# Kernel optimization log

Measured on AMD Instinct MI355X. Metric: run time of the kernel, lower is better.

## Reference

```python
import jax, jax.numpy as jnp
import numpy as np

N_HEAD, CTX, N_EMBD, HEAD_SIZE = 16, 2048, 1024, 64
D_MODEL = N_HEAD * HEAD_SIZE  # 1024


def setup_inputs() -> dict:
    key = jax.random.key(0)
    ks = jax.random.split(key, 8)
    s_in = 1.0 / np.sqrt(N_EMBD)
    s_d = 1.0 / np.sqrt(D_MODEL)
    s_ff = 1.0 / np.sqrt(4 * D_MODEL)
    return {
        "x": jax.random.normal(ks[0], (4, CTX, N_EMBD), dtype=jnp.float32),
        # per-head q/k/v projections stacked over heads: [H, n_embd, head_size]
        "Wq": jax.random.normal(ks[1], (N_HEAD, N_EMBD, HEAD_SIZE), dtype=jnp.float32) * s_in,
        "Wk": jax.random.normal(ks[2], (N_HEAD, N_EMBD, HEAD_SIZE), dtype=jnp.float32) * s_in,
        "Wv": jax.random.normal(ks[3], (N_HEAD, N_EMBD, HEAD_SIZE), dtype=jnp.float32) * s_in,
        # FFN: Linear(d, 4d) -> Linear(4d, d) -> ReLU (dropout = identity in eval)
        "W1": jax.random.normal(ks[4], (D_MODEL, 4 * D_MODEL), dtype=jnp.float32) * s_d,
        "b1": jnp.zeros((4 * D_MODEL,), dtype=jnp.float32),
        "W2": jax.random.normal(ks[5], (4 * D_MODEL, D_MODEL), dtype=jnp.float32) * s_ff,
        "b2": jnp.zeros((D_MODEL,), dtype=jnp.float32),
    }


def reference(x, Wq, Wk, Wv, W1, b1, W2, b2):
    B, T, C = x.shape
    scale = 1.0 / np.sqrt(HEAD_SIZE)
    # project: [B,T,C] x [H,C,D] -> [B,H,T,D]
    q = jnp.einsum('btc,hcd->bhtd', x, Wq)
    k = jnp.einsum('btc,hcd->bhtd', x, Wk)
    v = jnp.einsum('btc,hcd->bhtd', x, Wv)
    # causal attention scores [B,H,T,T]
    wei = jnp.einsum('bhtd,bhsd->bhts', q, k) * scale
    causal = jnp.tril(jnp.ones((T, T), dtype=bool))
    wei = jnp.where(causal, wei, -jnp.inf)
    wei = jax.nn.softmax(wei, axis=-1)
    out = jnp.einsum('bhts,bhsd->bhtd', wei, v)
    # concat heads -> [B,T,H*D]
    out = out.transpose(0, 2, 1, 3).reshape(B, T, D_MODEL)
    # FFN: note original applies ReLU AFTER the second linear
    h = out @ W1 + b1
    h = h @ W2 + b2
    return jax.nn.relu(h)
```

## Files before the change

kernel.cpp:

```cpp
#include <hip/hip_runtime.h>
#include <hip/hip_bf16.h>

typedef unsigned short u16;
typedef unsigned int u32;
typedef short bf16x8 __attribute__((ext_vector_type(8)));
typedef float floatx4 __attribute__((ext_vector_type(4)));

#define CTX 2048
#define HEADSZ 64
#define NHEAD 16
#define DMODEL 1024
#define DFF 4096
#define MROWS 8192
#define C_SCALE 0.18033688011112042f

__device__ __forceinline__ u16 f2b(float f) {
  union { float f; u32 i; } x; x.f = f;
  u32 i = x.i;
  return (u16)((i + 0x7fffu + ((i >> 16) & 1u)) >> 16);
}
__device__ __forceinline__ u32 pack2(float a, float b) {
  return (u32)f2b(a) | ((u32)f2b(b) << 16);
}
__device__ __forceinline__ u32 cvtpk(float a, float b) {
  u32 r;
  asm("v_cvt_pk_bf16_f32 %0, %1, %2" : "=v"(r) : "v"(a), "v"(b));
  return r;
}

__device__ __forceinline__ void gl2lds16(const u16* g, u16* l) {
  __builtin_amdgcn_global_load_lds(
      (const __attribute__((address_space(1))) void*)g,
      (__attribute__((address_space(3))) void*)l, 16, 0, 0);
}

__global__ __launch_bounds__(256) void cvt_f32_bf16(const float* __restrict__ in,
                                                    u16* __restrict__ out) {
  int i = (blockIdx.x * 256 + threadIdx.x) * 4;
  float4 v = *(const float4*)(in + i);
  *(uint2*)(out + i) = make_uint2(pack2(v.x, v.y), pack2(v.z, v.w));
}

__global__ void transpose_f32_bf16(const float* __restrict__ in, u16* __restrict__ out,
                                   int R, int C, long ibs, long obs) {
  __shared__ u16 tile[32][33];
  const float* ip = in + (size_t)blockIdx.z * ibs;
  u16* op = out + (size_t)blockIdx.z * obs;
  int c0 = blockIdx.x * 32, r0 = blockIdx.y * 32;
  int tx = threadIdx.x, ty = threadIdx.y;
#pragma unroll
  for (int i = 0; i < 32; i += 8)
    tile[ty + i][tx] = f2b(ip[(size_t)(r0 + ty + i) * C + (c0 + tx)]);
  __syncthreads();
#pragma unroll
  for (int i = 0; i < 32; i += 8)
    op[(size_t)(c0 + ty + i) * R + (r0 + tx)] = tile[tx][ty + i];
}

__global__ void transpose_qkv(const float* __restrict__ Wq, const float* __restrict__ Wk,
                              const float* __restrict__ Wv, u16* __restrict__ out) {
  __shared__ u16 tile[32][33];
  int z = blockIdx.z;
  int sec = z >> 4, hh = z & 15;
  const float* ip = (sec == 0 ? Wq : sec == 1 ? Wk : Wv) + (size_t)hh * 65536;
  u16* op = out + (size_t)(sec * 16 + hh) * 65536;
  int c0 = blockIdx.x * 32, r0 = blockIdx.y * 32;
  int tx = threadIdx.x, ty = threadIdx.y;
#pragma unroll
  for (int i = 0; i < 32; i += 8)
    tile[ty + i][tx] = f2b(ip[(size_t)(r0 + ty + i) * 64 + (c0 + tx)]);
  __syncthreads();
#pragma unroll
  for (int i = 0; i < 32; i += 8)
    op[(size_t)(c0 + ty + i) * 1024 + (r0 + tx)] = tile[tx][ty + i];
}

__global__ __launch_bounds__(256) void reduce_wf(const float* __restrict__ p,
                                                 u16* __restrict__ wft) {
  int i = (blockIdx.x * 256 + threadIdx.x) * 4;
  float4 s = *(const float4*)(p + i);
#pragma unroll
  for (int sp = 1; sp < 8; sp++) {
    float4 v = *(const float4*)(p + ((size_t)sp << 20) + i);
    s.x += v.x; s.y += v.y; s.z += v.z; s.w += v.w;
  }
  *(uint2*)(wft + i) = make_uint2(pack2(s.x, s.y), pack2(s.z, s.w));
}

__global__ __launch_bounds__(256) void bf_init(const float* __restrict__ b2,
                                               float* __restrict__ bf) {
  int n = blockIdx.x * 256 + threadIdx.x;
  bf[n] = b2[n];
}
__global__ __launch_bounds__(256) void bf_acc(const float* __restrict__ b1,
                                              const float* __restrict__ W2,
                                              float* __restrict__ bf) {
  int n = blockIdx.x * 256 + threadIdx.x;
  int f0 = blockIdx.y * 128;
  float s = 0.f;
  for (int f = 0; f < 128; f++) s += b1[f0 + f] * W2[(size_t)(f0 + f) * 1024 + n];
  atomicAdd(&bf[n], s);
}

template <int MODE>
__global__ __launch_bounds__(512, 2) void gemm128(
    const u16* __restrict__ A, const u16* __restrict__ Bt,
    const float* __restrict__ bias,
    void* __restrict__ o0v, void* __restrict__ o1v, void* __restrict__ o2v,
    int N, int Klen, int Kstride) {
  __shared__ __align__(16) u16 As[3][8192];
  __shared__ __align__(16) u16 Bs[3][16384];
  const int tid = threadIdx.x;
  const int quad = (tid >> 4) & 3, l15 = tid & 15;
  const int wave = tid >> 6;
  const int wr = wave >> 2, wc = wave & 3;

  const int id = blockIdx.x;
  int blockM, blockN, koff;
  if (MODE == 3) {
    blockM = (id & 7) << 7;
    blockN = ((id >> 3) & 3) << 8;
    koff = (id >> 5) << 9;
  } else {
    blockM = (((id & 7) << 3) | ((id >> 3) & 7)) << 7;
    blockN = (id >> 6) << 8;
    koff = 0;
  }

  const int sub = tid >> 3;
  const int kslot = (tid & 7) ^ (sub & 7);
  const int rA = blockM + ((sub >> 5) << 6) + (sub & 31);
  const u16* a0 = A + (size_t)(rA + 0) * Kstride + koff + kslot * 8;
  const u16* a1 = A + (size_t)(rA + 32) * Kstride + koff + kslot * 8;
  const int rB = blockN + sub;
  const u16* b0 = Bt + (size_t)(rB + 0) * Kstride + koff + kslot * 8;
  const u16* b1 = Bt + (size_t)(rB + 64) * Kstride + koff + kslot * 8;
  const u16* b2 = Bt + (size_t)(rB + 128) * Kstride + koff + kslot * 8;
  const u16* b3 = Bt + (size_t)(rB + 192) * Kstride + koff + kslot * 8;

  const int arow = ((wr << 5) + l15) << 7;
  const int brow = ((wc << 6) + l15) << 7;
  const int swz0 = (quad ^ (l15 & 7)) << 4;
  const int swz1 = ((4 + quad) ^ (l15 & 7)) << 4;

  floatx4 acc[4][4];
#pragma unroll
  for (int i = 0; i < 4; i++)
#pragma unroll
    for (int j = 0; j < 4; j++) acc[i][j] = (floatx4){0.f, 0.f, 0.f, 0.f};

  const int nk = Klen >> 6;

  gl2lds16(a0, &As[0][tid * 8]);
  gl2lds16(a1, &As[0][4096 + tid * 8]);
  gl2lds16(b0, &Bs[0][0 * 4096 + tid * 8]);
  gl2lds16(b1, &Bs[0][1 * 4096 + tid * 8]);
  gl2lds16(b2, &Bs[0][2 * 4096 + tid * 8]);
  gl2lds16(b3, &Bs[0][3 * 4096 + tid * 8]);
  gl2lds16(a0 + 64, &As[1][tid * 8]);
  gl2lds16(a1 + 64, &As[1][4096 + tid * 8]);
  gl2lds16(b0 + 64, &Bs[1][0 * 4096 + tid * 8]);
  gl2lds16(b1 + 64, &Bs[1][1 * 4096 + tid * 8]);
  gl2lds16(b2 + 64, &Bs[1][2 * 4096 + tid * 8]);
  gl2lds16(b3 + 64, &Bs[1][3 * 4096 + tid * 8]);
  asm volatile("s_waitcnt vmcnt(6)" ::: "memory");
  __builtin_amdgcn_s_barrier();
  a0 += 128; a1 += 128;
  b0 += 128; b1 += 128; b2 += 128; b3 += 128;

#define MFMA_Q(q, arq)                                                         \
  _Pragma("unroll") for (int nf = 0; nf < 4; nf++)                             \
    acc[q][nf] = __builtin_amdgcn_mfma_f32_16x16x32_bf16(                      \
        arq[0], br[nf][0], acc[q][nf], 0, 0, 0);                               \
  _Pragma("unroll") for (int nf = 0; nf < 4; nf++)                             \
    acc[q][nf] = __builtin_amdgcn_mfma_f32_16x16x32_bf16(                      \
        arq[1], br[nf][1], acc[q][nf], 0, 0, 0);

  int cur = 0;
#pragma unroll 1
  for (int t = 0; t < nk; t++) {
    const char* ab = (const char*)As[cur];
    const char* bb = (const char*)Bs[cur];
    int nxt = cur + 2; if (nxt >= 3) nxt -= 3;
    u16* An = As[nxt];
    u16* Bn = Bs[nxt];
    const bool st2 = (t + 2 < nk);
    bf16x8 br[4][2], ar0[2], ar1[2], ar2[2], ar3[2];

#pragma unroll
    for (int nf = 0; nf < 4; nf++) {
      br[nf][0] = *(const bf16x8*)(bb + nf * 2048 + brow + swz0);
      br[nf][1] = *(const bf16x8*)(bb + nf * 2048 + brow + swz1);
    }
    ar0[0] = *(const bf16x8*)(ab + arow + swz0);
    ar0[1] = *(const bf16x8*)(ab + arow + swz1);
    ar1[0] = *(const bf16x8*)(ab + 2048 + arow + swz0);
    ar1[1] = *(const bf16x8*)(ab + 2048 + arow + swz1);
    if (st2) {
      gl2lds16(a0, An + tid * 8);
      gl2lds16(a1, An + 4096 + tid * 8);
      gl2lds16(b0, Bn + 0 * 4096 + tid * 8);
      gl2lds16(b1, Bn + 1 * 4096 + tid * 8);
      gl2lds16(b2, Bn + 2 * 4096 + tid * 8);
      gl2lds16(b3, Bn + 3 * 4096 + tid * 8);
    }
    __builtin_amdgcn_s_barrier();
    asm volatile("s_waitcnt lgkmcnt(0)" ::: "memory");
    __builtin_amdgcn_s_setprio(1);
    MFMA_Q(0, ar0)
    MFMA_Q(1, ar1)
    __builtin_amdgcn_s_setprio(0);
    __builtin_amdgcn_s_barrier();

    ar2[0] = *(const bf16x8*)(ab + 8192 + arow + swz0);
    ar2[1] = *(const bf16x8*)(ab + 8192 + arow + swz1);
    ar3[0] = *(const bf16x8*)(ab + 8192 + 2048 + arow + swz0);
    ar3[1] = *(const bf16x8*)(ab + 8192 + 2048 + arow + swz1);
    __builtin_amdgcn_s_barrier();
    asm volatile("s_waitcnt lgkmcnt(0)" ::: "memory");
    __builtin_amdgcn_s_setprio(1);
    MFMA_Q(2, ar2)
    MFMA_Q(3, ar3)
    __builtin_amdgcn_s_setprio(0);
    if (st2)
      asm volatile("s_waitcnt vmcnt(6)" ::: "memory");
    else
      asm volatile("s_waitcnt vmcnt(0)" ::: "memory");
    __builtin_amdgcn_s_barrier();

    a0 += 64; a1 += 64;
    b0 += 64; b1 += 64; b2 += 64; b3 += 64;
    cur = (cur == 2) ? 0 : cur + 1;
  }
#undef MFMA_Q

  const int m0 = blockM + wr * 64 + quad * 4;
  const int n0 = blockN + wc * 64 + l15;
  if (MODE == 0) {
    u16* o0 = (u16*)o0v; u16* o1 = (u16*)o1v; u16* o2 = (u16*)o2v;
    const int lane = tid & 63;
    const int n0w = blockN + wc * 64;
    const int sec = n0w >> 10, hh = (n0w >> 6) & 15;
    const int m0w = blockM + wr * 64;
    const int b = m0w >> 11, t0 = m0w & 2047;
    const int lr = lane >> 3, lc = lane & 7;
    u16* buf = (u16*)Bs[0] + wave * 4096;
    if (sec < 2) {
      u16* dst = (sec == 0) ? o0 : o1;
      const float scl = (sec == 0) ? C_SCALE : 1.0f;
#pragma unroll
      for (int nf = 0; nf < 4; nf++)
#pragma unroll
        for (int mf = 0; mf < 4; mf++)
#pragma unroll
          for (int r = 0; r < 4; r++) {
            int row = mf * 16 + quad * 4 + r;
            int col2 = (nf * 16 + l15) ^ ((row & 7) << 3);
            buf[row * 64 + col2] = f2b(acc[mf][nf][r] * scl);
          }
      u16* base = dst + ((size_t)((b * 16 + hh) * 2048 + t0)) * 64 + lc * 8;
#pragma unroll
      for (int i = 0; i < 8; i++) {
        int row = i * 8 + lr;
        uint4 v = *(const uint4*)(buf + row * 64 + ((lc ^ lr) << 3));
        *(uint4*)(base + (size_t)row * 64) = v;
      }
    } else {
      u16* dstv = o2 + ((size_t)((b * 16 + hh) * 64)) * CTX + t0;
#pragma unroll
      for (int nf = 0; nf < 4; nf++)
#pragma unroll
        for (int mf = 0; mf < 4; mf++) {
          int dr = nf * 16 + l15;
          int tc = (mf * 16 + quad * 4) ^ ((dr & 7) << 3);
          *(uint2*)&buf[dr * 64 + tc] = make_uint2(
              pack2(acc[mf][nf][0], acc[mf][nf][1]),
              pack2(acc[mf][nf][2], acc[mf][nf][3]));
        }
#pragma unroll
      for (int i = 0; i < 8; i++) {
        int dr = i * 8 + lr;
        uint4 v = *(const uint4*)&buf[dr * 64 + ((lc * 8) ^ ((dr & 7) << 3))];
        *(uint4*)(dstv + (size_t)dr * CTX + lc * 8) = v;
      }
    }
  } else if (MODE == 2) {
    float* o0 = (float*)o0v;
#pragma unroll
    for (int nf = 0; nf < 4; nf++) {
      int n = n0 + nf * 16;
      float bv = bias[n];
#pragma unroll
      for (int mf = 0; mf < 4; mf++)
#pragma unroll
        for (int r = 0; r < 4; r++) {
          int m = m0 + mf * 16 + r;
          float v = acc[mf][nf][r] + bv;
          o0[(size_t)m * N + n] = v > 0.f ? v : 0.f;
        }
    }
  } else {
    float* o0 = (float*)o0v + ((size_t)(id >> 5) << 20);
#pragma unroll
    for (int nf = 0; nf < 4; nf++) {
      int n = n0 + nf * 16;
#pragma unroll
      for (int mf = 0; mf < 4; mf++)
#pragma unroll
        for (int r = 0; r < 4; r++) {
          int m = m0 + mf * 16 + r;
          o0[(size_t)m * N + n] = acc[mf][nf][r];
        }
    }
  }
}

__global__ __launch_bounds__(256) void attn_mfma(
    const u16* __restrict__ Q, const u16* __restrict__ K,
    const u16* __restrict__ Vt, u16* __restrict__ out) {
  __shared__ __align__(16) u16 Kbuf[2][4096];
  __shared__ __align__(16) u16 Vbuf[2][4096];
  __shared__ __align__(16) u16 Plds[4][32][72];
  const int tid = threadIdx.x;
  const int wave = tid >> 6, lane = tid & 63;
  const int quad = lane >> 4, l15 = lane & 15;
  const int sx = l15 & 7;
  const int bh = blockIdx.x;
  const int j = 15 - blockIdx.y;
  const size_t qkb = (size_t)bh * CTX * 64;
  const size_t vb = (size_t)bh * 64 * CTX;

  const int ch0 = wave * 64 + lane;
  const int ch1 = 256 + ch0;
  const int r0 = ch0 >> 3, s0 = (ch0 & 7) ^ (r0 & 7);
  const int r1 = ch1 >> 3, s1 = (ch1 & 7) ^ (r1 & 7);
  const u16* kg0 = K + qkb + r0 * 64 + s0 * 8;
  const u16* kg1 = K + qkb + r1 * 64 + s1 * 8;
  const u16* vg0 = Vt + vb + (size_t)r0 * CTX + s0 * 8;
  const u16* vg1 = Vt + vb + (size_t)r1 * CTX + s1 * 8;

  const int qbase = j * 128 + wave * 32;
  const int NST = 2 * j + 2;
  const int nstw = 2 * j + (wave >> 1) + 1;

  bf16x8 qf[2][2];
#pragma unroll
  for (int mt = 0; mt < 2; mt++)
#pragma unroll
    for (int kc = 0; kc < 2; kc++)
      qf[mt][kc] = *(const bf16x8*)(Q + qkb + (size_t)(qbase + mt * 16 + l15) * 64 + kc * 32 + quad * 8);

  bf16x8 ones;
#pragma unroll
  for (int i = 0; i < 8; i++) ones[i] = (short)0x3F80;

  floatx4 o[2][4];
#pragma unroll
  for (int mt = 0; mt < 2; mt++)
#pragma unroll
    for (int dt = 0; dt < 4; dt++) o[mt][dt] = (floatx4){0.f, 0.f, 0.f, 0.f};
  floatx4 lacc[2];
  lacc[0] = (floatx4){0.f, 0.f, 0.f, 0.f};
  lacc[1] = (floatx4){0.f, 0.f, 0.f, 0.f};

  gl2lds16(kg0, &Kbuf[0][wave * 512]);
  gl2lds16(kg1, &Kbuf[0][2048 + wave * 512]);
  gl2lds16(vg0, &Vbuf[0][wave * 512]);
  gl2lds16(vg1, &Vbuf[0][2048 + wave * 512]);

#pragma unroll 1
  for (int st = 0; st < NST; st++) {
    __syncthreads();
    if (st + 1 < NST) {
      const int sb = (st + 1) * 64;
      const int b = (st + 1) & 1;
      gl2lds16(kg0 + sb * 64, &Kbuf[b][wave * 512]);
      gl2lds16(kg1 + sb * 64, &Kbuf[b][2048 + wave * 512]);
      gl2lds16(vg0 + sb, &Vbuf[b][wave * 512]);
      gl2lds16(vg1 + sb, &Vbuf[b][2048 + wave * 512]);
    }
    if (st >= nstw) continue;
    const int sbase = st * 64;
    const u16* kb = Kbuf[st & 1];
    const u16* vv = Vbuf[st & 1];

    floatx4 stf[2][4];
    __builtin_amdgcn_s_setprio(1);
#pragma unroll
    for (int sc = 0; sc < 4; sc++) {
      const bf16x8* kr = (const bf16x8*)(kb + (sc * 16 + l15) * 64);
      bf16x8 k0 = kr[quad ^ sx];
      bf16x8 k1 = kr[(4 + quad) ^ sx];
#pragma unroll
      for (int mt = 0; mt < 2; mt++) {
        floatx4 z = (floatx4){0.f, 0.f, 0.f, 0.f};
        z = __builtin_amdgcn_mfma_f32_16x16x32_bf16(k0, qf[mt][0], z, 0, 0, 0);
        stf[mt][sc] = __builtin_amdgcn_mfma_f32_16x16x32_bf16(k1, qf[mt][1], z, 0, 0, 0);
      }
    }
    __builtin_amdgcn_s_setprio(0);
    if (st == nstw - 1) {
#pragma unroll
      for (int mt = 0; mt < 2; mt++) {
        int qq = qbase + mt * 16 + l15;
#pragma unroll
        for (int sc = 0; sc < 4; sc++)
#pragma unroll
          for (int r = 0; r < 4; r++) {
            int s = sbase + sc * 16 + quad * 4 + r;
            if (s > qq) stf[mt][sc][r] = -1e30f;
          }
      }
    }
#pragma unroll
    for (int mt = 0; mt < 2; mt++) {
#pragma unroll
      for (int sc = 0; sc < 4; sc++) {
        floatx4 s4 = stf[mt][sc];
        float p0 = exp2f(s4[0]);
        float p1 = exp2f(s4[1]);
        float p2 = exp2f(s4[2]);
        float p3 = exp2f(s4[3]);
        *(uint2*)&Plds[wave][mt * 16 + l15][sc * 16 + quad * 4] =
            make_uint2(cvtpk(p0, p1), cvtpk(p2, p3));
      }
    }
    asm volatile("s_waitcnt lgkmcnt(0)" ::: "memory");
    __builtin_amdgcn_s_setprio(1);
#pragma unroll
    for (int sc2 = 0; sc2 < 2; sc2++) {
      bf16x8 pf[2];
#pragma unroll
      for (int mt = 0; mt < 2; mt++)
        pf[mt] = *(const bf16x8*)&Plds[wave][mt * 16 + l15][sc2 * 32 + quad * 8];
#pragma unroll
      for (int mt = 0; mt < 2; mt++)
        lacc[mt] = __builtin_amdgcn_mfma_f32_16x16x32_bf16(ones, pf[mt], lacc[mt], 0, 0, 0);
#pragma unroll
      for (int dt = 0; dt < 4; dt++) {
        const bf16x8* vr = (const bf16x8*)(vv + (dt * 16 + l15) * 64);
        bf16x8 vf = vr[(sc2 * 4 + quad) ^ sx];
#pragma unroll
        for (int mt = 0; mt < 2; mt++)
          o[mt][dt] = __builtin_amdgcn_mfma_f32_16x16x32_bf16(vf, pf[mt], o[mt][dt], 0, 0, 0);
      }
    }
    __builtin_amdgcn_s_setprio(0);
  }

#pragma unroll
  for (int mt = 0; mt < 2; mt++) {
    float inv = 1.0f / lacc[mt][0];
    int row = (bh >> 4) * CTX + qbase + mt * 16 + l15;
    u16* orow = out + (size_t)row * DMODEL + (bh & 15) * 64;
#pragma unroll
    for (int dt = 0; dt < 4; dt++) {
      floatx4 v = o[mt][dt];
      *(u32*)(orow + dt * 16 + quad * 4) = cvtpk(v[0] * inv, v[1] * inv);
      *(u32*)(orow + dt * 16 + quad * 4 + 2) = cvtpk(v[2] * inv, v[3] * inv);
    }
  }
}

extern "C" void kernel_launch(void* const* d_in, const int* in_sizes, int n_in,
                              void* d_out, int out_size, void* d_ws, size_t ws_size,
                              hipStream_t stream) {
  const float* x  = (const float*)d_in[0];
  const float* Wq = (const float*)d_in[1];
  const float* Wk = (const float*)d_in[2];
  const float* Wv = (const float*)d_in[3];
  const float* W1 = (const float*)d_in[4];
  const float* b1 = (const float*)d_in[5];
  const float* W2 = (const float*)d_in[6];
  const float* b2 = (const float*)d_in[7];
  float* out = (float*)d_out;

  u16* ws    = (u16*)d_ws;
  u16* W2t   = ws;
  u16* W1b   = W2t + (size_t)1024 * 4096;
  u16* Wft   = W1b + (size_t)1024 * 4096;
  float* bfv = (float*)(Wft + (size_t)1024 * 1024);
  u16* xb    = Wft + (size_t)1024 * 1024 + 4096;
  u16* Wqkvt = xb + (size_t)MROWS * 1024;
  u16* q     = Wqkvt + (size_t)3072 * 1024;
  u16* k     = q + (size_t)MROWS * 1024;
  u16* vt    = k + (size_t)MROWS * 1024;
  u16* att   = xb;
  float* partials = (float*)q;

  cvt_f32_bf16<<<MROWS * 1024 / 1024, 256, 0, stream>>>(x, xb);
  cvt_f32_bf16<<<1024 * 4096 / 1024, 256, 0, stream>>>(W1, W1b);

  dim3 tb(32, 8);
  transpose_qkv<<<dim3(2, 32, 48), tb, 0, stream>>>(Wq, Wk, Wv, Wqkvt);
  transpose_f32_bf16<<<dim3(32, 128, 1), tb, 0, stream>>>(W2, W2t, 4096, 1024, 0, 0);

  gemm128<3><<<256, 512, 0, stream>>>(W2t, W1b, nullptr, partials, nullptr, nullptr,
                                      1024, 512, 4096);
  reduce_wf<<<1024, 256, 0, stream>>>(partials, Wft);
  bf_init<<<4, 256, 0, stream>>>(b2, bfv);
  bf_acc<<<dim3(4, 32), 256, 0, stream>>>(b1, W2, bfv);

  gemm128<0><<<768, 512, 0, stream>>>(xb, Wqkvt, nullptr, q, k, vt, 3072, 1024, 1024);
  attn_mfma<<<dim3(64, 16), 256, 0, stream>>>(q, k, vt, att);
  gemm128<2><<<256, 512, 0, stream>>>(att, Wft, bfv, out, nullptr, nullptr,
                                      1024, 1024, 1024);
}
```

Before: 330.7 us.

## Shrink GEMM LDS to double-buffered K=32 tiles and merge small launches

```diff
diff --git a/kernel.cpp b/kernel.cpp
--- a/kernel.cpp
+++ b/kernel.cpp
@@ -34,11 +34,19 @@
       (__attribute__((address_space(3))) void*)l, 16, 0, 0);
 }
 
-__global__ __launch_bounds__(256) void cvt_f32_bf16(const float* __restrict__ in,
-                                                    u16* __restrict__ out) {
+__global__ __launch_bounds__(256) void cvt2(const float* __restrict__ x,
+                                            u16* __restrict__ xb,
+                                            const float* __restrict__ w1,
+                                            u16* __restrict__ w1b) {
   int i = (blockIdx.x * 256 + threadIdx.x) * 4;
-  float4 v = *(const float4*)(in + i);
-  *(uint2*)(out + i) = make_uint2(pack2(v.x, v.y), pack2(v.z, v.w));
+  if (i < MROWS * 1024) {
+    float4 v = *(const float4*)(x + i);
+    *(uint2*)(xb + i) = make_uint2(pack2(v.x, v.y), pack2(v.z, v.w));
+  } else {
+    int j = i - MROWS * 1024;
+    float4 v = *(const float4*)(w1 + j);
+    *(uint2*)(w1b + j) = make_uint2(pack2(v.x, v.y), pack2(v.z, v.w));
+  }
 }
 
 __global__ void transpose_f32_bf16(const float* __restrict__ in, u16* __restrict__ out,
@@ -87,11 +95,6 @@
   *(uint2*)(wft + i) = make_uint2(pack2(s.x, s.y), pack2(s.z, s.w));
 }
 
-__global__ __launch_bounds__(256) void bf_init(const float* __restrict__ b2,
-                                               float* __restrict__ bf) {
-  int n = blockIdx.x * 256 + threadIdx.x;
-  bf[n] = b2[n];
-}
 __global__ __launch_bounds__(256) void bf_acc(const float* __restrict__ b1,
                                               const float* __restrict__ W2,
                                               float* __restrict__ bf) {
@@ -103,13 +106,12 @@
 }
 
 template <int MODE>
-__global__ __launch_bounds__(512, 2) void gemm128(
+__global__ __launch_bounds__(512, 4) void gemm128(
     const u16* __restrict__ A, const u16* __restrict__ Bt,
     const float* __restrict__ bias,
     void* __restrict__ o0v, void* __restrict__ o1v, void* __restrict__ o2v,
     int N, int Klen, int Kstride) {
-  __shared__ __align__(16) u16 As[3][8192];
-  __shared__ __align__(16) u16 Bs[3][16384];
+  __shared__ __align__(16) u16 SH[32768];
   const int tid = threadIdx.x;
   const int quad = (tid >> 4) & 3, l15 = tid & 15;
   const int wave = tid >> 6;
@@ -127,21 +129,11 @@
     koff = 0;
   }
 
-  const int sub = tid >> 3;
-  const int kslot = (tid & 7) ^ (sub & 7);
-  const int rA = blockM + ((sub >> 5) << 6) + (sub & 31);
-  const u16* a0 = A + (size_t)(rA + 0) * Kstride + koff + kslot * 8;
-  const u16* a1 = A + (size_t)(rA + 32) * Kstride + koff + kslot * 8;
-  const int rB = blockN + sub;
-  const u16* b0 = Bt + (size_t)(rB + 0) * Kstride + koff + kslot * 8;
-  const u16* b1 = Bt + (size_t)(rB + 64) * Kstride + koff + kslot * 8;
-  const u16* b2 = Bt + (size_t)(rB + 128) * Kstride + koff + kslot * 8;
-  const u16* b3 = Bt + (size_t)(rB + 192) * Kstride + koff + kslot * 8;
-
-  const int arow = ((wr << 5) + l15) << 7;
-  const int brow = ((wc << 6) + l15) << 7;
-  const int swz0 = (quad ^ (l15 & 7)) << 4;
-  const int swz1 = ((4 + quad) ^ (l15 & 7)) << 4;
+  const int crow = tid >> 2;
+  const int cslot = (tid & 3) ^ (crow & 3);
+  const u16* ap  = A + (size_t)(blockM + crow) * Kstride + koff + cslot * 8;
+  const u16* bp0 = Bt + (size_t)(blockN + crow) * Kstride + koff + cslot * 8;
+  const u16* bp1 = bp0 + (size_t)128 * Kstride;
 
   floatx4 acc[4][4];
 #pragma unroll
@@ -149,90 +141,50 @@
 #pragma unroll
     for (int j = 0; j < 4; j++) acc[i][j] = (floatx4){0.f, 0.f, 0.f, 0.f};
 
-  const int nk = Klen >> 6;
-
-  gl2lds16(a0, &As[0][tid * 8]);
-  gl2lds16(a1, &As[0][4096 + tid * 8]);
-  gl2lds16(b0, &Bs[0][0 * 4096 + tid * 8]);
-  gl2lds16(b1, &Bs[0][1 * 4096 + tid * 8]);
-  gl2lds16(b2, &Bs[0][2 * 4096 + tid * 8]);
-  gl2lds16(b3, &Bs[0][3 * 4096 + tid * 8]);
-  gl2lds16(a0 + 64, &As[1][tid * 8]);
-  gl2lds16(a1 + 64, &As[1][4096 + tid * 8]);
-  gl2lds16(b0 + 64, &Bs[1][0 * 4096 + tid * 8]);
-  gl2lds16(b1 + 64, &Bs[1][1 * 4096 + tid * 8]);
-  gl2lds16(b2 + 64, &Bs[1][2 * 4096 + tid * 8]);
-  gl2lds16(b3 + 64, &Bs[1][3 * 4096 + tid * 8]);
-  asm volatile("s_waitcnt vmcnt(6)" ::: "memory");
-  __builtin_amdgcn_s_barrier();
-  a0 += 128; a1 += 128;
-  b0 += 128; b1 += 128; b2 += 128; b3 += 128;
-
-#define MFMA_Q(q, arq)                                                         \
-  _Pragma("unroll") for (int nf = 0; nf < 4; nf++)                             \
-    acc[q][nf] = __builtin_amdgcn_mfma_f32_16x16x32_bf16(                      \
-        arq[0], br[nf][0], acc[q][nf], 0, 0, 0);                               \
-  _Pragma("unroll") for (int nf = 0; nf < 4; nf++)                             \
-    acc[q][nf] = __builtin_amdgcn_mfma_f32_16x16x32_bf16(                      \
-        arq[1], br[nf][1], acc[q][nf], 0, 0, 0);
-
-  int cur = 0;
+  const int nk = Klen >> 5;
+
+  gl2lds16(ap, SH + tid * 8);
+  gl2lds16(bp0, SH + 8192 + tid * 8);
+  gl2lds16(bp1, SH + 8192 + 4096 + tid * 8);
+  ap += 32; bp0 += 32; bp1 += 32;
+
+  const int aoff = (wr * 64 + l15) * 64 + ((quad ^ (l15 & 3)) << 4);
+  const int boff = (wc * 64 + l15) * 64 + ((quad ^ (l15 & 3)) << 4);
+
 #pragma unroll 1
   for (int t = 0; t < nk; t++) {
-    const char* ab = (const char*)As[cur];
-    const char* bb = (const char*)Bs[cur];
-    int nxt = cur + 2; if (nxt >= 3) nxt -= 3;
-    u16* An = As[nxt];
-    u16* Bn = Bs[nxt];
-    const bool st2 = (t + 2 < nk);
-    bf16x8 br[4][2], ar0[2], ar1[2], ar2[2], ar3[2];
-
-#pragma unroll
-    for (int nf = 0; nf < 4; nf++) {
-      br[nf][0] = *(const bf16x8*)(bb + nf * 2048 + brow + swz0);
-      br[nf][1] = *(const bf16x8*)(bb + nf * 2048 + brow + swz1);
-    }
-    ar0[0] = *(const bf16x8*)(ab + arow + swz0);
-    ar0[1] = *(const bf16x8*)(ab + arow + swz1);
-    ar1[0] = *(const bf16x8*)(ab + 2048 + arow + swz0);
-    ar1[1] = *(const bf16x8*)(ab + 2048 + arow + swz1);
-    if (st2) {
-      gl2lds16(a0, An + tid * 8);
-      gl2lds16(a1, An + 4096 + tid * 8);
-      gl2lds16(b0, Bn + 0 * 4096 + tid * 8);
-      gl2lds16(b1, Bn + 1 * 4096 + tid * 8);
-      gl2lds16(b2, Bn + 2 * 4096 + tid * 8);
-      gl2lds16(b3, Bn + 3 * 4096 + tid * 8);
+    const int cur = t & 1, nxt = cur ^ 1;
+    if (t + 1 < nk) {
+      u16* An = SH + nxt * 4096;
+      u16* Bn = SH + 8192 + nxt * 8192;
+      gl2lds16(ap, An + tid * 8);
+      gl2lds16(bp0, Bn + tid * 8);
+      gl2lds16(bp1, Bn + 4096 + tid * 8);
+      ap += 32; bp0 += 32; bp1 += 32;
+      asm volatile("s_waitcnt vmcnt(3)" ::: "memory");
+    } else {
+      asm volatile("s_waitcnt vmcnt(0)" ::: "memory");
     }
     __builtin_amdgcn_s_barrier();
+    const char* ab = (const char*)(SH + cur * 4096);
+    const char* bb = (const char*)(SH + 8192 + cur * 8192);
+    bf16x8 ar[4], br[4];
+#pragma unroll
+    for (int mf = 0; mf < 4; mf++)
+      ar[mf] = *(const bf16x8*)(ab + mf * 1024 + aoff);
+#pragma unroll
+    for (int nf = 0; nf < 4; nf++)
+      br[nf] = *(const bf16x8*)(bb + nf * 1024 + boff);
     asm volatile("s_waitcnt lgkmcnt(0)" ::: "memory");
     __builtin_amdgcn_s_setprio(1);
-    MFMA_Q(0, ar0)
-    MFMA_Q(1, ar1)
+#pragma unroll
+    for (int mf = 0; mf < 4; mf++)
+#pragma unroll
+      for (int nf = 0; nf < 4; nf++)
+        acc[mf][nf] = __builtin_amdgcn_mfma_f32_16x16x32_bf16(ar[mf], br[nf], acc[mf][nf], 0, 0, 0);
     __builtin_amdgcn_s_setprio(0);
     __builtin_amdgcn_s_barrier();
-
-    ar2[0] = *(const bf16x8*)(ab + 8192 + arow + swz0);
-    ar2[1] = *(const bf16x8*)(ab + 8192 + arow + swz1);
-    ar3[0] = *(const bf16x8*)(ab + 8192 + 2048 + arow + swz0);
-    ar3[1] = *(const bf16x8*)(ab + 8192 + 2048 + arow + swz1);
-    __builtin_amdgcn_s_barrier();
-    asm volatile("s_waitcnt lgkmcnt(0)" ::: "memory");
-    __builtin_amdgcn_s_setprio(1);
-    MFMA_Q(2, ar2)
-    MFMA_Q(3, ar3)
-    __builtin_amdgcn_s_setprio(0);
-    if (st2)
-      asm volatile("s_waitcnt vmcnt(6)" ::: "memory");
-    else
-      asm volatile("s_waitcnt vmcnt(0)" ::: "memory");
-    __builtin_amdgcn_s_barrier();
-
-    a0 += 64; a1 += 64;
-    b0 += 64; b1 += 64; b2 += 64; b3 += 64;
-    cur = (cur == 2) ? 0 : cur + 1;
-  }
-#undef MFMA_Q
+  }
 
   const int m0 = blockM + wr * 64 + quad * 4;
   const int n0 = blockN + wc * 64 + l15;
@@ -244,7 +196,7 @@
     const int m0w = blockM + wr * 64;
     const int b = m0w >> 11, t0 = m0w & 2047;
     const int lr = lane >> 3, lc = lane & 7;
-    u16* buf = (u16*)Bs[0] + wave * 4096;
+    u16* buf = SH + wave * 4096;
     if (sec < 2) {
       u16* dst = (sec == 0) ? o0 : o1;
       const float scl = (sec == 0) ? C_SCALE : 1.0f;
@@ -286,10 +238,11 @@
     }
   } else if (MODE == 2) {
     float* o0 = (float*)o0v;
+    const float* bias2 = (const float*)o1v;
 #pragma unroll
     for (int nf = 0; nf < 4; nf++) {
       int n = n0 + nf * 16;
-      float bv = bias[n];
+      float bv = bias[n] + bias2[n];
 #pragma unroll
       for (int mf = 0; mf < 4; mf++)
 #pragma unroll
@@ -488,8 +441,7 @@
   u16* att   = xb;
   float* partials = (float*)q;
 
-  cvt_f32_bf16<<<MROWS * 1024 / 1024, 256, 0, stream>>>(x, xb);
-  cvt_f32_bf16<<<1024 * 4096 / 1024, 256, 0, stream>>>(W1, W1b);
+  cvt2<<<(MROWS * 1024 + 1024 * 4096) / 1024, 256, 0, stream>>>(x, xb, W1, W1b);
 
   dim3 tb(32, 8);
   transpose_qkv<<<dim3(2, 32, 48), tb, 0, stream>>>(Wq, Wk, Wv, Wqkvt);
@@ -498,11 +450,11 @@
   gemm128<3><<<256, 512, 0, stream>>>(W2t, W1b, nullptr, partials, nullptr, nullptr,
                                       1024, 512, 4096);
   reduce_wf<<<1024, 256, 0, stream>>>(partials, Wft);
-  bf_init<<<4, 256, 0, stream>>>(b2, bfv);
+  hipMemsetAsync(bfv, 0, 1024 * sizeof(float), stream);
   bf_acc<<<dim3(4, 32), 256, 0, stream>>>(b1, W2, bfv);
 
   gemm128<0><<<768, 512, 0, stream>>>(xb, Wqkvt, nullptr, q, k, vt, 3072, 1024, 1024);
   attn_mfma<<<dim3(64, 16), 256, 0, stream>>>(q, k, vt, att);
-  gemm128<2><<<256, 512, 0, stream>>>(att, Wft, bfv, out, nullptr, nullptr,
+  gemm128<2><<<256, 512, 0, stream>>>(att, Wft, bfv, out, (void*)b2, nullptr,
                                       1024, 1024, 1024);
 }
```

Result: faster. 312.9 us (-5.4%).
